# Optimization experiments

Measured on AMD Instinct MI355X. Metric: run time of the kernel, lower is better.

The kernel has to match this reference:

```python
import jax, jax.numpy as jnp
import numpy as np

B, S, D = 2, 2048, 2048
H, HD = 16, 128
F = 8192
LC = 512
EPS = 1e-6


def _linear_params(k, din, dout):
    k1, k2 = jax.random.split(k)
    w = jax.random.normal(k1, (din, dout), jnp.float32) * 0.02
    b = jax.random.normal(k2, (dout,), jnp.float32) * 0.02
    return w, b


def setup_inputs() -> dict:
    key = jax.random.key(0)
    ks = jax.random.split(key, 20)
    inp = {}
    inp["x"] = jax.random.normal(ks[0], (B, S, D), jnp.float32)
    inp["e"] = jax.random.normal(ks[1], (B, 6, D), jnp.float32) * 0.1
    inp["context"] = jax.random.normal(ks[2], (B, LC, D), jnp.float32)
    # per-token rotary angles [S, HD//2] (Wan builds such a table from 3D grid)
    inp["freqs"] = jax.random.uniform(ks[3], (S, HD // 2), jnp.float32) * (2.0 * np.pi)
    inp["modulation"] = jax.random.normal(ks[4], (1, 6, D), jnp.float32) / np.sqrt(D)
    names = ["sq", "sk", "sv", "so", "cq", "ck", "cv", "co"]
    for i, nm in enumerate(names):
        w, b = _linear_params(ks[5 + i], D, D)
        inp[nm + "_w"], inp[nm + "_b"] = w, b
    inp["f1_w"], inp["f1_b"] = _linear_params(ks[13], D, F)
    inp["f2_w"], inp["f2_b"] = _linear_params(ks[14], F, D)
    inp["snq"] = jnp.ones((D,), jnp.float32)
    inp["snk"] = jnp.ones((D,), jnp.float32)
    inp["cnq"] = jnp.ones((D,), jnp.float32)
    inp["cnk"] = jnp.ones((D,), jnp.float32)
    return inp


def _rmsnorm(x, w):
    # WanRMSNorm: x * rsqrt(mean(x^2) + eps) * weight
    return x * jax.lax.rsqrt(jnp.mean(x * x, axis=-1, keepdims=True) + EPS) * w


def _layernorm(x):
    # elementwise_affine=False LayerNorm
    m = jnp.mean(x, axis=-1, keepdims=True)
    v = jnp.mean((x - m) ** 2, axis=-1, keepdims=True)
    return (x - m) * jax.lax.rsqrt(v + EPS)


def _rope(x, ang):
    # x: [B, S, H, HD]; ang: [S, HD//2]; adjacent pairs rotated (view_as_complex)
    c = jnp.cos(ang)[None, :, None, :]
    s = jnp.sin(ang)[None, :, None, :]
    xr, xi = x[..., 0::2], x[..., 1::2]
    out = jnp.stack([xr * c - xi * s, xr * s + xi * c], axis=-1)
    return out.reshape(x.shape)


def _attn(q, k, v):
    # q: [B,Sq,H,HD], k/v: [B,Sk,H,HD] -> [B,Sq,H,HD]
    scores = jnp.einsum("bqhd,bkhd->bhqk", q, k) / np.sqrt(HD)
    probs = jax.nn.softmax(scores, axis=-1)
    return jnp.einsum("bhqk,bkhd->bqhd", probs, v)


def reference(x, e, context, freqs, modulation,
              sq_w, sq_b, sk_w, sk_b, sv_w, sv_b, so_w, so_b, snq, snk,
              cq_w, cq_b, ck_w, ck_b, cv_w, cv_b, co_w, co_b, cnq, cnk,
              f1_w, f1_b, f2_w, f2_b):
    em = modulation + e  # [B,6,D]
    e0, e1, e2, e3, e4, e5 = [em[:, i:i + 1, :] for i in range(6)]

    # self-attention with AdaLN modulation
    tx = _layernorm(x) * (1.0 + e1) + e0
    q = _rmsnorm(tx @ sq_w + sq_b, snq).reshape(B, S, H, HD)
    k = _rmsnorm(tx @ sk_w + sk_b, snk).reshape(B, S, H, HD)
    v = (tx @ sv_w + sv_b).reshape(B, S, H, HD)
    q, k = _rope(q, freqs), _rope(k, freqs)
    y = _attn(q, k, v).reshape(B, S, D) @ so_w + so_b
    x = x + y * e2

    # cross-attention (norm3 = Identity since cross_attn_norm=False)
    q = _rmsnorm(x @ cq_w + cq_b, cnq).reshape(B, S, H, HD)
    k = _rmsnorm(context @ ck_w + ck_b, cnk).reshape(B, LC, H, HD)
    v = (context @ cv_w + cv_b).reshape(B, LC, H, HD)
    x = x + (_attn(q, k, v).reshape(B, S, D) @ co_w + co_b)

    # FFN with AdaLN modulation
    tx = _layernorm(x) * (1.0 + e4) + e3
    y = jax.nn.gelu(tx @ f1_w + f1_b, approximate=True) @ f2_w + f2_b
    x = x + y * e5
    return x
```

## Files before the change

kernel.cpp:

```cpp
#include <hip/hip_runtime.h>
#include <hip/hip_bf16.h>

using bf16 = __hip_bfloat16;
typedef __attribute__((ext_vector_type(8))) short bf16x8;
typedef __attribute__((ext_vector_type(4))) float f32x4;
typedef const __attribute__((address_space(1))) unsigned int* gp_t;
typedef __attribute__((address_space(3))) unsigned int* sp_t;

#define B_   2
#define S_   2048
#define D_   2048
#define H_   16
#define HD_  128
#define F_   8192
#define LC_  512
#define ESTRIDE (6*D_)

__device__ __forceinline__ float bsum4(float v, float* rs) {
  #pragma unroll
  for (int o = 32; o; o >>= 1) v += __shfl_down(v, o, 64);
  int lane = threadIdx.x & 63, w = threadIdx.x >> 6;
  if (!lane) rs[w] = v;
  __syncthreads();
  float r = rs[0] + rs[1] + rs[2] + rs[3];
  __syncthreads();
  return r;
}
__device__ __forceinline__ float bmax4(float v, float* rs) {
  #pragma unroll
  for (int o = 32; o; o >>= 1) v = fmaxf(v, __shfl_down(v, o, 64));
  int lane = threadIdx.x & 63, w = threadIdx.x >> 6;
  if (!lane) rs[w] = v;
  __syncthreads();
  float r = fmaxf(fmaxf(rs[0], rs[1]), fmaxf(rs[2], rs[3]));
  __syncthreads();
  return r;
}

__global__ void k_addmod(const float* __restrict__ e, const float* __restrict__ mod,
                         float* __restrict__ em) {
  int i = blockIdx.x * 256 + threadIdx.x;
  em[i] = e[i] + mod[i % (6 * D_)];
}

__global__ void k_f2b(const float* __restrict__ in, bf16* __restrict__ out) {
  int i = blockIdx.x * 256 + threadIdx.x;
  out[i] = __float2bfloat16(in[i]);
}

__global__ void k_copy_f32(const float* __restrict__ in, float* __restrict__ out) {
  int i = blockIdx.x * 256 + threadIdx.x;
  out[i] = in[i];
}

__global__ void k_tr_f2b(const float* __restrict__ in, bf16* __restrict__ out,
                         int K, int N) {
  __shared__ float tile[64][65];
  int kb = blockIdx.y << 6, nb = blockIdx.x << 6;
  int x = threadIdx.x & 63, y = threadIdx.x >> 6;
  #pragma unroll
  for (int r = y; r < 64; r += 4) tile[r][x] = in[(size_t)(kb + r) * N + nb + x];
  __syncthreads();
  #pragma unroll
  for (int r = y; r < 64; r += 4)
    out[(size_t)(nb + r) * K + kb + x] = __float2bfloat16(tile[x][r]);
}

__global__ void k_tr_b2b(const bf16* __restrict__ in, bf16* __restrict__ out,
                         int R, int C, long long sIn, long long sOut) {
  in  += (long long)blockIdx.z * sIn;
  out += (long long)blockIdx.z * sOut;
  __shared__ bf16 tile[64][65];
  int rb = blockIdx.y << 6, cb = blockIdx.x << 6;
  int x = threadIdx.x & 63, y = threadIdx.x >> 6;
  #pragma unroll
  for (int r = y; r < 64; r += 4) tile[r][x] = in[(size_t)(rb + r) * C + cb + x];
  __syncthreads();
  #pragma unroll
  for (int r = y; r < 64; r += 4) out[(size_t)(cb + r) * R + rb + x] = tile[x][r];
}

__global__ void k_ln_mod(const float* __restrict__ x, const float* __restrict__ em,
                         int i0, int i1, bf16* __restrict__ out, int s_per_b) {
  __shared__ float rs[4];
  int row = blockIdx.x, t = threadIdx.x;
  int b = row / s_per_b;
  const float* xr = x + (size_t)row * D_;
  float vals[8], s = 0.f, ss = 0.f;
  #pragma unroll
  for (int j = 0; j < 8; j++) {
    float v = xr[t + j * 256];
    vals[j] = v; s += v; ss += v * v;
  }
  s  = bsum4(s, rs);
  ss = bsum4(ss, rs);
  float mean = s * (1.f / D_);
  float var  = ss * (1.f / D_) - mean * mean;
  float inv  = rsqrtf(var + 1e-6f);
  const float* e0 = em + ((size_t)b * 6 + i0) * D_;
  const float* e1 = em + ((size_t)b * 6 + i1) * D_;
  bf16* orow = out + (size_t)row * D_;
  #pragma unroll
  for (int j = 0; j < 8; j++) {
    int c = t + j * 256;
    orow[c] = __float2bfloat16((vals[j] - mean) * inv * (1.f + e1[c]) + e0[c]);
  }
}

__global__ void k_rms_rope(bf16* __restrict__ buf, const float* __restrict__ w,
                           const float* __restrict__ freqs, int do_rope, int s_per_b) {
  __shared__ float rs[4];
  int row = blockIdx.x, t = threadIdx.x;
  bf16* pr = buf + (size_t)row * D_;
  float4 raw = *(const float4*)(pr + (size_t)t * 8);
  bf16* hb = (bf16*)&raw;
  float v[8], ss = 0.f;
  #pragma unroll
  for (int j = 0; j < 8; j++) { v[j] = __bfloat162float(hb[j]); ss += v[j] * v[j]; }
  ss = bsum4(ss, rs);
  float inv = rsqrtf(ss * (1.f / D_) + 1e-6f);
  int base = t * 8;
  #pragma unroll
  for (int j = 0; j < 8; j++) v[j] = v[j] * inv * w[base + j];
  if (do_rope) {
    int s = row % s_per_b;
    const float* fr = freqs + (size_t)s * (HD_ / 2) + ((base & (HD_ - 1)) >> 1);
    #pragma unroll
    for (int p = 0; p < 4; p++) {
      float ang = fr[p];
      float c = cosf(ang), sn = sinf(ang);
      float xr = v[2 * p], xi = v[2 * p + 1];
      v[2 * p]     = xr * c - xi * sn;
      v[2 * p + 1] = xr * sn + xi * c;
    }
  }
  float4 ow; bf16* ho = (bf16*)&ow;
  #pragma unroll
  for (int j = 0; j < 8; j++) ho[j] = __float2bfloat16(v[j]);
  *(float4*)(pr + (size_t)t * 8) = ow;
}

template <int EPT>
__global__ void k_softmax(bf16* __restrict__ buf, int N) {
  __shared__ float rs[4];
  int row = blockIdx.x, t = threadIdx.x;
  bf16* pr = buf + (size_t)row * N;
  float v[EPT], mx = -1e30f;
  #pragma unroll
  for (int j = 0; j < EPT; j++) { v[j] = __bfloat162float(pr[t + j * 256]); mx = fmaxf(mx, v[j]); }
  mx = bmax4(mx, rs);
  float s = 0.f;
  #pragma unroll
  for (int j = 0; j < EPT; j++) { v[j] = __expf(v[j] - mx); s += v[j]; }
  s = bsum4(s, rs);
  float invs = 1.f / s;
  #pragma unroll
  for (int j = 0; j < EPT; j++) pr[t + j * 256] = __float2bfloat16(v[j] * invs);
}

template <int EPI>
__global__ __launch_bounds__(256) void gemm_bt(
    const bf16* __restrict__ A, int lda, long long sA,
    const bf16* __restrict__ Bt, int ldb, long long sB,
    const float* __restrict__ bias,
    bf16* __restrict__ Cb, int ldc, long long sCb,
    float* __restrict__ Cf, const float* __restrict__ Xin,
    float scale, const float* __restrict__ evec, int s_per_b,
    int K) {
  __shared__ __align__(16) bf16 As[128][32];
  __shared__ __align__(16) bf16 Bs[128][32];
  const int z = blockIdx.z;
  A  += (long long)z * sA;
  Bt += (long long)z * sB;
  const int m0 = blockIdx.y * 128, n0 = blockIdx.x * 128;
  const int t = threadIdx.x;
  const int w = t >> 6, lane = t & 63;
  const int wrow = (w >> 1) * 64, wcol = (w & 1) * 64;
  const int quad = lane >> 4, l16 = lane & 15;

  f32x4 zero = {0.f, 0.f, 0.f, 0.f};
  f32x4 acc[4][4];
  #pragma unroll
  for (int i = 0; i < 4; i++)
    #pragma unroll
    for (int j = 0; j < 4; j++) acc[i][j] = zero;

  for (int k0 = 0; k0 < K; k0 += 32) {
    #pragma unroll
    for (int i = 0; i < 2; i++) {
      int c = t + i * 256;
      int r = c >> 2, col = (c & 3) * 8;
      __builtin_amdgcn_global_load_lds(
          (gp_t)(A + (size_t)(m0 + r) * lda + k0 + col),
          (sp_t)(&As[0][0] + (size_t)(w * 64 + i * 256) * 8), 16, 0, 0);
      __builtin_amdgcn_global_load_lds(
          (gp_t)(Bt + (size_t)(n0 + r) * ldb + k0 + col),
          (sp_t)(&Bs[0][0] + (size_t)(w * 64 + i * 256) * 8), 16, 0, 0);
    }
    __syncthreads();
    bf16x8 af[4], bfr[4];
    #pragma unroll
    for (int mi = 0; mi < 4; mi++) af[mi]  = *(const bf16x8*)(&As[wrow + mi * 16 + l16][quad * 8]);
    #pragma unroll
    for (int ni = 0; ni < 4; ni++) bfr[ni] = *(const bf16x8*)(&Bs[wcol + ni * 16 + l16][quad * 8]);
    #pragma unroll
    for (int mi = 0; mi < 4; mi++)
      #pragma unroll
      for (int ni = 0; ni < 4; ni++)
        acc[mi][ni] = __builtin_amdgcn_mfma_f32_16x16x32_bf16(af[mi], bfr[ni], acc[mi][ni], 0, 0, 0);
    __syncthreads();
  }

  #pragma unroll
  for (int mi = 0; mi < 4; mi++) {
    #pragma unroll
    for (int r = 0; r < 4; r++) {
      int gm = m0 + wrow + mi * 16 + quad * 4 + r;
      #pragma unroll
      for (int ni = 0; ni < 4; ni++) {
        int gn = n0 + wcol + ni * 16 + l16;
        float v = acc[mi][ni][r];
        if (EPI == 0) {
          if (bias) v += bias[gn];
          Cb[(long long)z * sCb + (size_t)gm * ldc + gn] = __float2bfloat16(v);
        } else if (EPI == 1) {
          Cb[(long long)z * sCb + (size_t)gm * ldc + gn] = __float2bfloat16(v * scale);
        } else if (EPI == 3) {
          v += bias[gn];
          float g = 0.5f * v * (1.f + tanhf(0.7978845608028654f * (v + 0.044715f * v * v * v)));
          Cb[(long long)z * sCb + (size_t)gm * ldc + gn] = __float2bfloat16(g);
        } else {
          v += bias[gn];
          if (evec) v *= evec[(size_t)(gm / s_per_b) * ESTRIDE + gn];
          float o = Xin[(size_t)gm * ldc + gn] + v;
          Cf[(size_t)gm * ldc + gn] = o;
          if (Cb) Cb[(size_t)gm * ldc + gn] = __float2bfloat16(o);
        }
      }
    }
  }
}

extern "C" void kernel_launch(void* const* d_in, const int* in_sizes, int n_in,
                              void* d_out, int out_size, void* d_ws, size_t ws_size,
                              hipStream_t stream) {
  const float* x     = (const float*)d_in[0];
  const float* e     = (const float*)d_in[1];
  const float* ctx   = (const float*)d_in[2];
  const float* freqs = (const float*)d_in[3];
  const float* modu  = (const float*)d_in[4];
  const float* sq_w = (const float*)d_in[5];  const float* sq_b = (const float*)d_in[6];
  const float* sk_w = (const float*)d_in[7];  const float* sk_b = (const float*)d_in[8];
  const float* sv_w = (const float*)d_in[9];  const float* sv_b = (const float*)d_in[10];
  const float* so_w = (const float*)d_in[11]; const float* so_b = (const float*)d_in[12];
  const float* cq_w = (const float*)d_in[13]; const float* cq_b = (const float*)d_in[14];
  const float* ck_w = (const float*)d_in[15]; const float* ck_b = (const float*)d_in[16];
  const float* cv_w = (const float*)d_in[17]; const float* cv_b = (const float*)d_in[18];
  const float* co_w = (const float*)d_in[19]; const float* co_b = (const float*)d_in[20];
  const float* f1_w = (const float*)d_in[21]; const float* f1_b = (const float*)d_in[22];
  const float* f2_w = (const float*)d_in[23]; const float* f2_b = (const float*)d_in[24];
  const float* snq  = (const float*)d_in[25]; const float* snk  = (const float*)d_in[26];
  const float* cnq  = (const float*)d_in[27]; const float* cnk  = (const float*)d_in[28];
  float* out = (float*)d_out;

  const size_t MD = (size_t)B_ * S_ * D_;

  char* W = (char*)d_ws;
  size_t off = 0;
  auto alloc = [&](size_t bytes) -> char* {
    char* p = W + off; off += (bytes + 255) & ~(size_t)255; return p;
  };
  float* em  = (float*)alloc((size_t)B_ * 6 * D_ * 4);
  bf16* wT   = (bf16*)alloc((size_t)F_ * D_ * 2);
  bf16* vb   = (bf16*)alloc(MD * 2);
  bf16* tx   = (bf16*)alloc(MD * 2);
  bf16* qb   = (bf16*)alloc(MD * 2);
  bf16* kb   = (bf16*)alloc(MD * 2);
  bf16* vt   = (bf16*)alloc(MD * 2);
  bf16* attnout = (bf16*)alloc(MD * 2);
  bf16* ctxb = (bf16*)alloc((size_t)B_ * LC_ * D_ * 2);
  bf16* kc   = (bf16*)alloc((size_t)B_ * LC_ * D_ * 2);
  bf16* vc   = (bf16*)alloc((size_t)B_ * LC_ * D_ * 2);
  bf16* vtc  = (bf16*)alloc((size_t)B_ * LC_ * D_ * 2);
  bf16* scores8 = wT;
  bf16* scoresC = wT;
  bf16* mid = qb;
  if (off > ws_size) {
    k_copy_f32<<<(int)(MD / 256), 256, 0, stream>>>(x, out);
    return;
  }

  const float qk_scale = 0.08838834764831845f;

  k_addmod<<<(B_ * 6 * D_) / 256, 256, 0, stream>>>(e, modu, em);
  k_f2b<<<(B_ * LC_ * D_) / 256, 256, 0, stream>>>(ctx, ctxb);

  k_ln_mod<<<B_ * S_, 256, 0, stream>>>(x, em, 0, 1, tx, S_);
  k_tr_f2b<<<dim3(D_ / 64, D_ / 64), 256, 0, stream>>>(sq_w, wT, D_, D_);
  gemm_bt<0><<<dim3(16, 32, 1), 256, 0, stream>>>(tx, D_, 0, wT, D_, 0, sq_b,
      qb, D_, 0, nullptr, nullptr, 1.f, nullptr, S_, D_);
  k_tr_f2b<<<dim3(D_ / 64, D_ / 64), 256, 0, stream>>>(sk_w, wT, D_, D_);
  gemm_bt<0><<<dim3(16, 32, 1), 256, 0, stream>>>(tx, D_, 0, wT, D_, 0, sk_b,
      kb, D_, 0, nullptr, nullptr, 1.f, nullptr, S_, D_);
  k_tr_f2b<<<dim3(D_ / 64, D_ / 64), 256, 0, stream>>>(sv_w, wT, D_, D_);
  gemm_bt<0><<<dim3(16, 32, 1), 256, 0, stream>>>(tx, D_, 0, wT, D_, 0, sv_b,
      vb, D_, 0, nullptr, nullptr, 1.f, nullptr, S_, D_);
  k_rms_rope<<<B_ * S_, 256, 0, stream>>>(qb, snq, freqs, 1, S_);
  k_rms_rope<<<B_ * S_, 256, 0, stream>>>(kb, snk, freqs, 1, S_);
  k_tr_b2b<<<dim3(D_ / 64, S_ / 64, B_), 256, 0, stream>>>(vb, vt, S_, D_,
      (long long)S_ * D_, (long long)D_ * S_);

  for (int b = 0; b < B_; b++) {
    for (int hc = 0; hc < 2; hc++) {
      const int h0 = hc * 8;
      const bf16* Aq = qb + (size_t)b * S_ * D_ + h0 * HD_;
      const bf16* Bk = kb + (size_t)b * S_ * D_ + h0 * HD_;
      gemm_bt<1><<<dim3(16, 16, 8), 256, 0, stream>>>(Aq, D_, HD_, Bk, D_, HD_, nullptr,
          scores8, S_, (long long)S_ * S_, nullptr, nullptr, qk_scale, nullptr, S_, HD_);
      k_softmax<8><<<8 * S_, 256, 0, stream>>>(scores8, S_);
      const bf16* Bv = vt + ((size_t)b * D_ + h0 * HD_) * S_;
      gemm_bt<0><<<dim3(1, 16, 8), 256, 0, stream>>>(scores8, S_, (long long)S_ * S_,
          Bv, S_, (long long)HD_ * S_, nullptr,
          attnout + (size_t)b * S_ * D_ + h0 * HD_, D_, HD_,
          nullptr, nullptr, 1.f, nullptr, S_, S_);
    }
  }
  k_tr_f2b<<<dim3(D_ / 64, D_ / 64), 256, 0, stream>>>(so_w, wT, D_, D_);
  gemm_bt<2><<<dim3(16, 32, 1), 256, 0, stream>>>(attnout, D_, 0, wT, D_, 0, so_b,
      tx, D_, 0, out, x, 1.f, em + 2 * D_, S_, D_);

  k_tr_f2b<<<dim3(D_ / 64, D_ / 64), 256, 0, stream>>>(cq_w, wT, D_, D_);
  gemm_bt<0><<<dim3(16, 32, 1), 256, 0, stream>>>(tx, D_, 0, wT, D_, 0, cq_b,
      qb, D_, 0, nullptr, nullptr, 1.f, nullptr, S_, D_);
  k_rms_rope<<<B_ * S_, 256, 0, stream>>>(qb, cnq, nullptr, 0, S_);
  k_tr_f2b<<<dim3(D_ / 64, D_ / 64), 256, 0, stream>>>(ck_w, wT, D_, D_);
  gemm_bt<0><<<dim3(16, 8, 1), 256, 0, stream>>>(ctxb, D_, 0, wT, D_, 0, ck_b,
      kc, D_, 0, nullptr, nullptr, 1.f, nullptr, S_, D_);
  k_rms_rope<<<B_ * LC_, 256, 0, stream>>>(kc, cnk, nullptr, 0, S_);
  k_tr_f2b<<<dim3(D_ / 64, D_ / 64), 256, 0, stream>>>(cv_w, wT, D_, D_);
  gemm_bt<0><<<dim3(16, 8, 1), 256, 0, stream>>>(ctxb, D_, 0, wT, D_, 0, cv_b,
      vc, D_, 0, nullptr, nullptr, 1.f, nullptr, S_, D_);
  k_tr_b2b<<<dim3(D_ / 64, LC_ / 64, B_), 256, 0, stream>>>(vc, vtc, LC_, D_,
      (long long)LC_ * D_, (long long)D_ * LC_);

  for (int b = 0; b < B_; b++) {
    gemm_bt<1><<<dim3(4, 16, 16), 256, 0, stream>>>(qb + (size_t)b * S_ * D_, D_, HD_,
        kc + (size_t)b * LC_ * D_, D_, HD_, nullptr,
        scoresC, LC_, (long long)S_ * LC_, nullptr, nullptr, qk_scale, nullptr, S_, HD_);
    k_softmax<2><<<16 * S_, 256, 0, stream>>>(scoresC, LC_);
    gemm_bt<0><<<dim3(1, 16, 16), 256, 0, stream>>>(scoresC, LC_, (long long)S_ * LC_,
        vtc + (size_t)b * D_ * LC_, LC_, (long long)HD_ * LC_, nullptr,
        attnout + (size_t)b * S_ * D_, D_, HD_, nullptr, nullptr, 1.f, nullptr, S_, LC_);
  }
  k_tr_f2b<<<dim3(D_ / 64, D_ / 64), 256, 0, stream>>>(co_w, wT, D_, D_);
  gemm_bt<2><<<dim3(16, 32, 1), 256, 0, stream>>>(attnout, D_, 0, wT, D_, 0, co_b,
      nullptr, D_, 0, out, out, 1.f, nullptr, S_, D_);

  k_ln_mod<<<B_ * S_, 256, 0, stream>>>(out, em, 3, 4, tx, S_);
  k_tr_f2b<<<dim3(F_ / 64, D_ / 64), 256, 0, stream>>>(f1_w, wT, D_, F_);
  gemm_bt<3><<<dim3(64, 32, 1), 256, 0, stream>>>(tx, D_, 0, wT, D_, 0, f1_b,
      mid, F_, 0, nullptr, nullptr, 1.f, nullptr, S_, D_);
  k_tr_f2b<<<dim3(D_ / 64, F_ / 64), 256, 0, stream>>>(f2_w, wT, F_, D_);
  gemm_bt<2><<<dim3(16, 32, 1), 256, 0, stream>>>(mid, F_, 0, wT, F_, 0, f2_b,
      nullptr, D_, 0, out, out, 1.f, em + 5 * D_, S_, F_);
}
```

Measured before the change: 1.919 ms.

## Add XCD-aware block swizzle and 64x64 GEMM for attention PV products

Remaps GEMM block indices so consecutive tiles that share operands land on the same XCD, aiming to improve L2 reuse across the chiplets. Also adds a smaller 64x64-tile GEMM kernel for the probs@V products, whose output is only 128 columns wide. The old kernel launched just 128 or 256 blocks there, so the new one raises the block count fourfold to fill more CUs. The trade-off is less register-level reuse per block and a kernel with no software pipelining.

```diff
diff --git a/kernel.cpp b/kernel.cpp
--- a/kernel.cpp
+++ b/kernel.cpp
@@ -156,6 +156,19 @@
   float invs = 1.f / s;
   #pragma unroll
   for (int j = 0; j < EPT; j++) pr[t + j * 256] = __float2bfloat16(v[j] * invs);
+}
+
+__device__ __forceinline__ void xcd_swizzle(int& bx, int& by) {
+  int nx = gridDim.x, ny = gridDim.y;
+  if ((nx & 7) == 0) {
+    int flat = by * nx + bx;
+    int xcd = flat & 7;
+    int idx = flat >> 3;
+    int sx = nx >> 3;
+    bx = xcd * sx + (idx % sx);
+    by = idx / sx;
+    (void)ny;
+  }
 }
 
 template <int EPI>
@@ -172,7 +185,9 @@
   const int z = blockIdx.z;
   A  += (long long)z * sA;
   Bt += (long long)z * sB;
-  const int m0 = blockIdx.y * 128, n0 = blockIdx.x * 128;
+  int bx = blockIdx.x, by = blockIdx.y;
+  xcd_swizzle(bx, by);
+  const int m0 = by * 128, n0 = bx * 128;
   const int t = threadIdx.x;
   const int w = t >> 6, lane = t & 63;
   const int wrow = (w >> 1) * 64, wcol = (w & 1) * 64;
@@ -241,6 +256,67 @@
   }
 }
 
+__global__ __launch_bounds__(256) void gemm64(
+    const bf16* __restrict__ A, int lda, long long sA,
+    const bf16* __restrict__ Bt, int ldb, long long sB,
+    bf16* __restrict__ Cb, int ldc, long long sCb,
+    int K) {
+  __shared__ __align__(16) bf16 As[64][32];
+  __shared__ __align__(16) bf16 Bs[64][32];
+  const int z = blockIdx.z;
+  A  += (long long)z * sA;
+  Bt += (long long)z * sB;
+  const int m0 = blockIdx.y * 64, n0 = blockIdx.x * 64;
+  const int t = threadIdx.x;
+  const int w = t >> 6, lane = t & 63;
+  const int wrow = (w >> 1) * 32, wcol = (w & 1) * 32;
+  const int quad = lane >> 4, l16 = lane & 15;
+
+  f32x4 zero = {0.f, 0.f, 0.f, 0.f};
+  f32x4 acc[2][2];
+  #pragma unroll
+  for (int i = 0; i < 2; i++)
+    #pragma unroll
+    for (int j = 0; j < 2; j++) acc[i][j] = zero;
+
+  for (int k0 = 0; k0 < K; k0 += 32) {
+    {
+      int r = t >> 2, col = (t & 3) * 8;
+      __builtin_amdgcn_global_load_lds(
+          (gp_t)(A + (size_t)(m0 + r) * lda + k0 + col),
+          (sp_t)(&As[0][0] + (size_t)(w * 64) * 8), 16, 0, 0);
+      __builtin_amdgcn_global_load_lds(
+          (gp_t)(Bt + (size_t)(n0 + r) * ldb + k0 + col),
+          (sp_t)(&Bs[0][0] + (size_t)(w * 64) * 8), 16, 0, 0);
+    }
+    __syncthreads();
+    bf16x8 af[2], bfr[2];
+    #pragma unroll
+    for (int mi = 0; mi < 2; mi++) af[mi]  = *(const bf16x8*)(&As[wrow + mi * 16 + l16][quad * 8]);
+    #pragma unroll
+    for (int ni = 0; ni < 2; ni++) bfr[ni] = *(const bf16x8*)(&Bs[wcol + ni * 16 + l16][quad * 8]);
+    #pragma unroll
+    for (int mi = 0; mi < 2; mi++)
+      #pragma unroll
+      for (int ni = 0; ni < 2; ni++)
+        acc[mi][ni] = __builtin_amdgcn_mfma_f32_16x16x32_bf16(af[mi], bfr[ni], acc[mi][ni], 0, 0, 0);
+    __syncthreads();
+  }
+
+  #pragma unroll
+  for (int mi = 0; mi < 2; mi++) {
+    #pragma unroll
+    for (int r = 0; r < 4; r++) {
+      int gm = m0 + wrow + mi * 16 + quad * 4 + r;
+      #pragma unroll
+      for (int ni = 0; ni < 2; ni++) {
+        int gn = n0 + wcol + ni * 16 + l16;
+        Cb[(long long)z * sCb + (size_t)gm * ldc + gn] = __float2bfloat16(acc[mi][ni][r]);
+      }
+    }
+  }
+}
+
 extern "C" void kernel_launch(void* const* d_in, const int* in_sizes, int n_in,
                               void* d_out, int out_size, void* d_ws, size_t ws_size,
                               hipStream_t stream) {
@@ -319,10 +395,9 @@
           scores8, S_, (long long)S_ * S_, nullptr, nullptr, qk_scale, nullptr, S_, HD_);
       k_softmax<8><<<8 * S_, 256, 0, stream>>>(scores8, S_);
       const bf16* Bv = vt + ((size_t)b * D_ + h0 * HD_) * S_;
-      gemm_bt<0><<<dim3(1, 16, 8), 256, 0, stream>>>(scores8, S_, (long long)S_ * S_,
-          Bv, S_, (long long)HD_ * S_, nullptr,
-          attnout + (size_t)b * S_ * D_ + h0 * HD_, D_, HD_,
-          nullptr, nullptr, 1.f, nullptr, S_, S_);
+      gemm64<<<dim3(2, 32, 8), 256, 0, stream>>>(scores8, S_, (long long)S_ * S_,
+          Bv, S_, (long long)HD_ * S_,
+          attnout + (size_t)b * S_ * D_ + h0 * HD_, D_, HD_, S_);
     }
   }
   k_tr_f2b<<<dim3(D_ / 64, D_ / 64), 256, 0, stream>>>(so_w, wT, D_, D_);
@@ -348,9 +423,9 @@
         kc + (size_t)b * LC_ * D_, D_, HD_, nullptr,
         scoresC, LC_, (long long)S_ * LC_, nullptr, nullptr, qk_scale, nullptr, S_, HD_);
     k_softmax<2><<<16 * S_, 256, 0, stream>>>(scoresC, LC_);
-    gemm_bt<0><<<dim3(1, 16, 16), 256, 0, stream>>>(scoresC, LC_, (long long)S_ * LC_,
-        vtc + (size_t)b * D_ * LC_, LC_, (long long)HD_ * LC_, nullptr,
-        attnout + (size_t)b * S_ * D_, D_, HD_, nullptr, nullptr, 1.f, nullptr, S_, LC_);
+    gemm64<<<dim3(2, 32, 16), 256, 0, stream>>>(scoresC, LC_, (long long)S_ * LC_,
+        vtc + (size_t)b * D_ * LC_, LC_, (long long)HD_ * LC_,
+        attnout + (size_t)b * S_ * D_, D_, HD_, LC_);
   }
   k_tr_f2b<<<dim3(D_ / 64, D_ / 64), 256, 0, stream>>>(co_w, wT, D_, D_);
   gemm_bt<2><<<dim3(16, 32, 1), 256, 0, stream>>>(attnout, D_, 0, wT, D_, 0, co_b,
```

Result: faster. 1.860 ms (-3.1%).
